# Kernel tuning notes

Hardware: AMD Instinct MI355X
Metric: run time of the kernel (lower is better)

The kernel has to match this reference:

```python
import jax, jax.numpy as jnp
import numpy as np

N = 4096   # out_features (rows of W)
M = 4096   # in_features (cols of W)
S_L = 2048 # Givens pairs on rows
S_R = 2048 # Givens pairs on cols
T = 8192   # tokens (batch*seq)
EPS = 1e-6


def _disjoint_pairs(key, n_feat, n_pairs):
    perm = jax.random.permutation(key, n_feat)[: 2 * n_pairs]
    return perm.reshape(n_pairs, 2).astype(jnp.int32)


def setup_inputs() -> dict:
    key = jax.random.key(0)
    ks = jax.random.split(key, 8)
    x = jax.random.normal(ks[0], (T, M), dtype=jnp.float32)
    W = 0.02 * jax.random.normal(ks[1], (N, M), dtype=jnp.float32)
    bias = jnp.zeros((N,), dtype=jnp.float32)
    theta_L = 0.002 * jax.random.normal(ks[2], (S_L,), dtype=jnp.float32)
    theta_R = 0.002 * jax.random.normal(ks[3], (S_R,), dtype=jnp.float32)
    pairs_L = _disjoint_pairs(ks[4], N, S_L)
    pairs_R = _disjoint_pairs(ks[5], M, S_R)
    ecd_log_mag = jnp.zeros((N,), dtype=jnp.float32)
    base_row_norms = jnp.linalg.norm(W, axis=1)  # [N], captured at init
    return {"x": x, "W": W, "bias": bias, "theta_L": theta_L,
            "theta_R": theta_R, "ecd_log_mag": ecd_log_mag,
            "base_row_norms": base_row_norms, "pairs_L": pairs_L,
            "pairs_R": pairs_R}


def _rotate_rows(Wm, pairs, theta):
    # Disjoint Givens rotations on rows: gather pair rows, 2x2 rotate, scatter.
    i, j = pairs[:, 0], pairs[:, 1]
    c = jnp.cos(theta)[:, None]
    s = jnp.sin(theta)[:, None]
    ri, rj = Wm[i], Wm[j]              # [S, M] gathers
    return Wm.at[i].set(c * ri - s * rj).at[j].set(s * ri + c * rj)


def _rotate_cols(Wm, pairs, theta):
    i, j = pairs[:, 0], pairs[:, 1]
    c = jnp.cos(theta)[None, :]
    s = jnp.sin(theta)[None, :]
    ci, cj = Wm[:, i], Wm[:, j]        # [N, S] gathers
    return Wm.at[:, i].set(c * ci - s * cj).at[:, j].set(s * ci + c * cj)


def reference(x, W, bias, theta_L, theta_R, ecd_log_mag, base_row_norms,
              pairs_L, pairs_R):
    # Effective weight: W_eff = G_L(theta_L) @ W @ G_R(theta_R)^T
    W_eff = _rotate_rows(_rotate_cols(W, pairs_R, theta_R), pairs_L, theta_L)
    # Magnitude (ECD) rescaling: restore base per-row norms modulated by
    # learned log-magnitudes.
    row_norms = jnp.sqrt(jnp.sum(W_eff * W_eff, axis=1) + EPS)  # [N]
    scale = base_row_norms * jnp.exp(ecd_log_mag) / row_norms   # [N]
    W_eff = W_eff * scale[:, None]
    return x @ W_eff.T + bias
```

## Files before the change

### kernel.cpp

```cpp
#include <hip/hip_runtime.h>
#include <cstdint>
#include <cstddef>

constexpr int T_N = 8192;
constexpr int MM  = 4096;
constexpr int NN  = 4096;
constexpr int S_L = 2048;
constexpr int S_R = 2048;
constexpr float EPS_ = 1e-6f;

typedef float  f32x4   __attribute__((ext_vector_type(4)));
typedef __bf16 bf16x8  __attribute__((ext_vector_type(8)));
typedef unsigned short ushort8 __attribute__((ext_vector_type(8)));

__device__ __forceinline__ unsigned short f2bf(float f) {
  unsigned int u = __float_as_uint(f);
  u += 0x7FFFu + ((u >> 16) & 1u);
  return (unsigned short)(u >> 16);
}

__global__ void init_cols(float* colC, float* colS, int* colP) {
  int i = blockIdx.x * blockDim.x + threadIdx.x;
  if (i < MM) { colC[i] = 1.f; colS[i] = 0.f; colP[i] = i; }
}

__global__ void build_cols(const float* __restrict__ thR, const int* __restrict__ prR,
                           float* colC, float* colS, int* colP) {
  int s = blockIdx.x * blockDim.x + threadIdx.x;
  if (s < S_R) {
    int i = prR[2*s], j = prR[2*s+1];
    float c = cosf(thR[s]), sn = sinf(thR[s]);
    colC[i] = c; colS[i] = -sn; colP[i] = j;
    colC[j] = c; colS[j] =  sn; colP[j] = i;
  }
}

__global__ __launch_bounds__(256) void weff_conv(
    const float* __restrict__ W, const float* __restrict__ brn, const float* __restrict__ elm,
    const float* __restrict__ thL, const int* __restrict__ prL,
    const float* __restrict__ colC, const float* __restrict__ colS, const int* __restrict__ colP,
    unsigned short* __restrict__ Wb,
    const float* __restrict__ x, unsigned short* __restrict__ xb)
{
  __shared__ __align__(16) float rI[MM];
  __shared__ __align__(16) float rJ[MM];
  __shared__ float red[8];

  int bid = blockIdx.x;
  int tid = threadIdx.x;

  if (bid >= S_L) {
    const size_t total = (size_t)T_N * MM / 8;
    for (size_t i = (size_t)(bid - S_L) * 256 + tid; i < total; i += 2048ull * 256ull) {
      const float* s = x + i * 8;
      f32x4 v0 = *(const f32x4*)s;
      f32x4 v1 = *(const f32x4*)(s + 4);
      ushort8 p;
      p[0] = f2bf(v0.x); p[1] = f2bf(v0.y); p[2] = f2bf(v0.z); p[3] = f2bf(v0.w);
      p[4] = f2bf(v1.x); p[5] = f2bf(v1.y); p[6] = f2bf(v1.z); p[7] = f2bf(v1.w);
      *(ushort8*)(xb + i * 8) = p;
    }
    return;
  }

  int s = bid;
  int i = prL[2*s], j = prL[2*s+1];
  float cl = cosf(thL[s]), sl = sinf(thL[s]);
  const float* Wi = W + (size_t)i * MM;
  const float* Wj = W + (size_t)j * MM;

  for (int m = tid * 4; m < MM; m += 1024) {
    *(f32x4*)&rI[m] = *(const f32x4*)&Wi[m];
    *(f32x4*)&rJ[m] = *(const f32x4*)&Wj[m];
  }
  __syncthreads();

  float ssi = 0.f, ssj = 0.f;
  for (int m = tid; m < MM; m += 256) {
    int p = colP[m];
    float c = colC[m], sn = colS[m];
    float vi = c * rI[m] + sn * rI[p];
    float vj = c * rJ[m] + sn * rJ[p];
    float ei = cl * vi - sl * vj;
    float ej = sl * vi + cl * vj;
    ssi += ei * ei;
    ssj += ej * ej;
  }
  #pragma unroll
  for (int o = 32; o; o >>= 1) { ssi += __shfl_xor(ssi, o); ssj += __shfl_xor(ssj, o); }
  int lane = tid & 63, wid = tid >> 6;
  if (lane == 0) { red[wid] = ssi; red[4 + wid] = ssj; }
  __syncthreads();
  float ti = red[0] + red[1] + red[2] + red[3];
  float tj = red[4] + red[5] + red[6] + red[7];
  float sci = brn[i] * expf(elm[i]) / sqrtf(ti + EPS_);
  float scj = brn[j] * expf(elm[j]) / sqrtf(tj + EPS_);

  for (int m0 = tid * 8; m0 < MM; m0 += 2048) {
    ushort8 pi, pj;
    #pragma unroll
    for (int q = 0; q < 8; q++) {
      int m = m0 + q;
      int p = colP[m];
      float c = colC[m], sn = colS[m];
      float vi = c * rI[m] + sn * rI[p];
      float vj = c * rJ[m] + sn * rJ[p];
      pi[q] = f2bf((cl * vi - sl * vj) * sci);
      pj[q] = f2bf((sl * vi + cl * vj) * scj);
    }
    *(ushort8*)&Wb[(size_t)i * MM + m0] = pi;
    *(ushort8*)&Wb[(size_t)j * MM + m0] = pj;
  }
}

typedef const __attribute__((address_space(1))) unsigned int* as1_u32p;
typedef __attribute__((address_space(3))) unsigned int* as3_u32p;

__device__ __forceinline__ void gl_lds16(const void* g, void* l) {
  __builtin_amdgcn_global_load_lds((as1_u32p)g, (as3_u32p)l, 16, 0, 0);
}

constexpr int GBM = 256, GBN = 256, GBK = 64;
constexpr int NTK = MM / GBK;
constexpr int BUFB = GBM * GBK * 2;

#define SB0() __builtin_amdgcn_sched_barrier(0)
#define BAR() __builtin_amdgcn_s_barrier()
#define LGKM(N) do { asm volatile("s_waitcnt lgkmcnt(" #N ")" ::: "memory"); \
                     SB0(); } while (0)

#define RD_A8(DST, AB, MIH)                                                   \
  _Pragma("unroll") for (int i_ = 0; i_ < 4; ++i_)                            \
  _Pragma("unroll") for (int k_ = 0; k_ < 2; ++k_)                            \
    DST[i_][k_] = *(const bf16x8*)((AB) + arow0 + ((MIH) * 4 + i_) * 2048     \
                                    + ((k_ * 64 + lg * 16) ^ sw));

#define RD_B4(DST, BB, NIH)                                                   \
  _Pragma("unroll") for (int n_ = 0; n_ < 2; ++n_)                            \
  _Pragma("unroll") for (int k_ = 0; k_ < 2; ++k_)                            \
    DST[n_][k_] = *(const bf16x8*)((BB) + brow0 + ((NIH) * 2 + n_) * 2048     \
                                    + ((k_ * 64 + lg * 16) ^ sw));

#define QMF(AF, BF, MI0, NI0)                                                 \
  __builtin_amdgcn_s_setprio(1);                                              \
  _Pragma("unroll") for (int k_ = 0; k_ < 2; ++k_)                            \
  _Pragma("unroll") for (int i_ = 0; i_ < 4; ++i_)                            \
  _Pragma("unroll") for (int n_ = 0; n_ < 2; ++n_)                            \
    acc[(MI0) + i_][(NI0) + n_] = __builtin_amdgcn_mfma_f32_16x16x32_bf16(    \
        AF[i_][k_], BF[n_][k_], acc[(MI0) + i_][(NI0) + n_], 0, 0, 0);        \
  __builtin_amdgcn_s_setprio(0);

#define STG_A(KOF, BUF, H)                                                    \
  _Pragma("unroll") for (int l_ = 2 * (H); l_ < 2 * (H) + 2; ++l_)            \
    gl_lds16(sA + (size_t)l_ * (64 * MM) + (KOF),                             \
             ldsA + (BUF) * BUFB + dstb + l_ * 8192);
#define STG_B(KOF, BUF, H)                                                    \
  _Pragma("unroll") for (int l_ = 2 * (H); l_ < 2 * (H) + 2; ++l_)            \
    gl_lds16(sB + (size_t)l_ * (64 * MM) + (KOF),                             \
             ldsB + (BUF) * BUFB + dstb + l_ * 8192);

#define GATE6  asm volatile("s_waitcnt vmcnt(6)" ::: "memory")
#define GATE0v asm volatile("s_waitcnt vmcnt(0)" ::: "memory")
#define GNONE  do { } while (0)
#define NOST   do { } while (0)

#define TILE4(T, BB, ST1, ST2, ST3, ST4, GATE)                                \
  {                                                                           \
    const char* Ab_ = ldsA + (BB) * BUFB;                                     \
    const char* Bb_ = ldsB + (BB) * BUFB;                                     \
    bf16x8 a0[4][2], a1[4][2], b0[2][2], b1[2][2];                            \
                          \
    RD_B4(b0, Bb_, 0);                                                        \
    RD_A8(a0, Ab_, 0);                                                        \
    SB0();                                                                    \
    ST1;                                                                      \
    LGKM(8);                                                                  \
    BAR();                                                                    \
    LGKM(0);                                                                  \
    QMF(a0, b0, 0, 0);                                                        \
    BAR();                                                                    \
                                    \
    RD_A8(a1, Ab_, 1);                                                        \
    SB0();                                                                    \
    ST2;                                                                      \
    BAR();                                                                    \
    LGKM(0);                                                                  \
    QMF(a1, b0, 4, 0);                                                        \
    BAR();                                                                    \
                                    \
    RD_B4(b1, Bb_, 1);                                                        \
    SB0();                                                                    \
    ST3;                                                                      \
    BAR();                                                                    \
    LGKM(0);                                                                  \
    QMF(a1, b1, 4, 2);                                                        \
    BAR();                                                                    \
                  \
    ST4;                                                                      \
    GATE;                                                                     \
    BAR();                                                                    \
    QMF(a0, b1, 0, 2);                                                        \
    BAR();                                                                    \
  }

__global__ __launch_bounds__(512, 2) void gemm8(
    const unsigned short* __restrict__ xb,
    const unsigned short* __restrict__ wb,
    const float* __restrict__ bias,
    float* __restrict__ C)
{
  __shared__ __align__(16) unsigned short As[2 * GBM * GBK];
  __shared__ __align__(16) unsigned short Bs[2 * GBN * GBK];
  char* ldsA = (char*)As;
  char* ldsB = (char*)Bs;

  int bid = blockIdx.x;
  int swz = (bid & 7) * 64 + (bid >> 3);
  int tn = swz & 15, tm = swz >> 4;
  const int trow0 = tm * GBM;
  const int tcol0 = tn * GBN;

  int tid  = threadIdx.x;
  int lane = tid & 63;
  int wid  = tid >> 6;
  int wr = wid >> 2, wc = wid & 3;
  int lr = lane & 15;
  int lg = lane >> 4;
  const int sw = (lr & 7) << 4;
  const int arow0 = (wr * 128 + lr) * 128;
  const int brow0 = (wc * 64  + lr) * 128;

  const int r0   = tid >> 3;
  const int colg = (tid & 7) ^ (r0 & 7);
  const unsigned short* sA = xb + (size_t)(trow0 + r0) * MM + colg * 8;
  const unsigned short* sB = wb + (size_t)(tcol0 + r0) * MM + colg * 8;
  const int dstb = tid * 16;

  f32x4 acc[8][4];
  #pragma unroll
  for (int i = 0; i < 8; i++)
    #pragma unroll
    for (int j = 0; j < 4; j++) {
      f32x4 z = {0.f, 0.f, 0.f, 0.f};
      acc[i][j] = z;
    }

  STG_A(0, 0, 0); STG_A(0, 0, 1); STG_B(0, 0, 0); STG_B(0, 0, 1);
  STG_A(GBK, 1, 0); STG_A(GBK, 1, 1); STG_B(GBK, 1, 0);
  asm volatile("s_waitcnt vmcnt(6)" ::: "memory");
  __builtin_amdgcn_s_barrier();

  #pragma unroll 1
  for (int t = 0; t < NTK - 2; t += 2) {
    TILE4(t, 0,
          STG_B((t + 1) * GBK, 1, 1),
          STG_A((t + 2) * GBK, 0, 0),
          STG_A((t + 2) * GBK, 0, 1),
          STG_B((t + 2) * GBK, 0, 0),
          GATE6);
    TILE4(t + 1, 1,
          STG_B((t + 2) * GBK, 0, 1),
          STG_A((t + 3) * GBK, 1, 0),
          STG_A((t + 3) * GBK, 1, 1),
          STG_B((t + 3) * GBK, 1, 0),
          GATE6);
  }
  TILE4(NTK - 2, 0,
        STG_B((NTK - 1) * GBK, 1, 1),
        NOST, NOST, NOST, GATE0v);
  TILE4(NTK - 1, 1, NOST, NOST, NOST, NOST, GNONE);

  #pragma unroll
  for (int ni = 0; ni < 4; ++ni) {
    int col = tcol0 + wc * 64 + ni * 16 + lr;
    float bi = bias[col];
    #pragma unroll
    for (int mi = 0; mi < 8; ++mi) {
      int rr0 = trow0 + wr * 128 + mi * 16 + lg * 4;
      #pragma unroll
      for (int qq = 0; qq < 4; ++qq)
        C[(size_t)(rr0 + qq) * NN + col] = acc[mi][ni][qq] + bi;
    }
  }
}

constexpr int BM = 128, BN = 128, BK = 64;

__global__ __launch_bounds__(256) void gemm_fb(
    const float* __restrict__ xf,
    const unsigned short* __restrict__ wb, const float* __restrict__ bias,
    float* __restrict__ C)
{
  __shared__ __align__(16) unsigned short As2[BM * BK];
  __shared__ __align__(16) unsigned short Bs2[BN * BK];

  int bid = blockIdx.x;
  int swz = (bid & 7) * 256 + (bid >> 3);
  int tn = swz & 31;
  int tm = swz >> 5;

  int tid  = threadIdx.x;
  int lane = tid & 63;
  int wid  = tid >> 6;
  int wr = wid >> 1, wc = wid & 1;
  int lr = lane & 15;
  int lg = lane >> 4;

  f32x4 acc[4][4];
  #pragma unroll
  for (int i = 0; i < 4; i++)
    #pragma unroll
    for (int j = 0; j < 4; j++) {
      f32x4 z = {0.f, 0.f, 0.f, 0.f};
      acc[i][j] = z;
    }

  int srow = tid >> 3;
  int scol = (tid & 7) * 8;
  const size_t a_base = (size_t)(tm * BM) * MM;
  const size_t b_base = (size_t)(tn * BN) * MM;

  for (int k0 = 0; k0 < MM; k0 += BK) {
    #pragma unroll
    for (int c = 0; c < 4; c++) {
      int row = c * 32 + srow;
      gl_lds16(wb + b_base + (size_t)row * MM + k0 + scol,
               (char*)Bs2 + (c * 256 + wid * 64) * 16);
    }
    #pragma unroll
    for (int c = 0; c < 4; c++) {
      int row = c * 32 + srow;
      const float* s = xf + a_base + (size_t)row * MM + k0 + scol;
      f32x4 v0 = *(const f32x4*)s;
      f32x4 v1 = *(const f32x4*)(s + 4);
      ushort8 p;
      p[0] = f2bf(v0.x); p[1] = f2bf(v0.y); p[2] = f2bf(v0.z); p[3] = f2bf(v0.w);
      p[4] = f2bf(v1.x); p[5] = f2bf(v1.y); p[6] = f2bf(v1.z); p[7] = f2bf(v1.w);
      *(ushort8*)&As2[(c * 256 + tid) * 8] = p;
    }
    __syncthreads();

    #pragma unroll
    for (int kk = 0; kk < 2; kk++) {
      bf16x8 a[4], b[4];
      #pragma unroll
      for (int i = 0; i < 4; i++) {
        a[i] = *(const bf16x8*)&As2[(wr * 64 + i * 16 + lr) * BK + kk * 32 + lg * 8];
        b[i] = *(const bf16x8*)&Bs2[(wc * 64 + i * 16 + lr) * BK + kk * 32 + lg * 8];
      }
      #pragma unroll
      for (int i = 0; i < 4; i++)
        #pragma unroll
        for (int j = 0; j < 4; j++)
          acc[i][j] = __builtin_amdgcn_mfma_f32_16x16x32_bf16(a[i], b[j], acc[i][j], 0, 0, 0);
    }
    __syncthreads();
  }

  int gn0 = tn * BN + wc * 64;
  int gt0 = tm * BM + wr * 64;
  #pragma unroll
  for (int j = 0; j < 4; j++) {
    int gn = gn0 + j * 16 + lr;
    float bi = bias[gn];
    #pragma unroll
    for (int i = 0; i < 4; i++) {
      int t0 = gt0 + i * 16 + lg * 4;
      #pragma unroll
      for (int q = 0; q < 4; q++)
        C[(size_t)(t0 + q) * NN + gn] = acc[i][j][q] + bi;
    }
  }
}

extern "C" void kernel_launch(void* const* d_in, const int* in_sizes, int n_in,
                              void* d_out, int out_size, void* d_ws, size_t ws_size,
                              hipStream_t stream)
{
  const float* x    = (const float*)d_in[0];
  const float* W    = (const float*)d_in[1];
  const float* bias = (const float*)d_in[2];
  const float* thL  = (const float*)d_in[3];
  const float* thR  = (const float*)d_in[4];
  const float* elm  = (const float*)d_in[5];
  const float* brn  = (const float*)d_in[6];
  const int*   prL  = (const int*)d_in[7];
  const int*   prR  = (const int*)d_in[8];
  float* out = (float*)d_out;

  char* ws = (char*)d_ws;
  unsigned short* Wb = (unsigned short*)ws;
  size_t off = (size_t)NN * MM * 2;
  float* colC = (float*)(ws + off); off += MM * 4;
  float* colS = (float*)(ws + off); off += MM * 4;
  int*   colP = (int*)  (ws + off); off += MM * 4;
  unsigned short* xb = (unsigned short*)(ws + off);
  bool use_xb = ws_size >= off + (size_t)T_N * MM * 2;

  init_cols <<<16, 256, 0, stream>>>(colC, colS, colP);
  build_cols<<< 8, 256, 0, stream>>>(thR, prR, colC, colS, colP);

  if (use_xb) {
    weff_conv<<<S_L + 2048, 256, 0, stream>>>(W, brn, elm, thL, prL,
                                              colC, colS, colP, Wb, x, xb);
    gemm8<<<512, 512, 0, stream>>>(xb, Wb, bias, out);
  } else {
    weff_conv<<<S_L, 256, 0, stream>>>(W, brn, elm, thL, prL,
                                       colC, colS, colP, Wb, x, xb);
    gemm_fb<<<2048, 256, 0, stream>>>(x, Wb, bias, out);
  }
}
```

Baseline: 302.0 us.

## Prefetch next tile's first A/B fragments during the current tile's MFMAs

Restructures the GEMM main loop so the a0/b0 LDS fragments for the next k-tile are read during the last MFMA phase of the current tile, using double-buffered register sets. LDS reads now overlap with MFMA work instead of stalling at the start of each tile. Global-to-LDS staging is reordered around this, and the vmcnt gate moves from 6 to 4. The cost is extra register pressure from holding two fragment sets, which could hurt occupancy at 2 waves per SIMD, plus more delicate ordering across the barriers.

```diff
diff --git a/kernel.cpp b/kernel.cpp
--- a/kernel.cpp
+++ b/kernel.cpp
@@ -126,7 +126,7 @@
 
 #define SB0() __builtin_amdgcn_sched_barrier(0)
 #define BAR() __builtin_amdgcn_s_barrier()
-#define LGKM(N) do { asm volatile("s_waitcnt lgkmcnt(" #N ")" ::: "memory"); \
+#define LGKM0() do { asm volatile("s_waitcnt lgkmcnt(0)" ::: "memory"); \
                      SB0(); } while (0)
 
 #define RD_A8(DST, AB, MIH)                                                   \
@@ -159,47 +159,41 @@
     gl_lds16(sB + (size_t)l_ * (64 * MM) + (KOF),                             \
              ldsB + (BUF) * BUFB + dstb + l_ * 8192);
 
-#define GATE6  asm volatile("s_waitcnt vmcnt(6)" ::: "memory")
-#define GATE0v asm volatile("s_waitcnt vmcnt(0)" ::: "memory")
+#define GATE4x asm volatile("s_waitcnt vmcnt(4)" ::: "memory")
+#define GATE0x asm volatile("s_waitcnt vmcnt(0)" ::: "memory")
 #define GNONE  do { } while (0)
-#define NOST   do { } while (0)
-
-#define TILE4(T, BB, ST1, ST2, ST3, ST4, GATE)                                \
+
+#define TILEX(T, BB, a0C, b0C, a0N, b0N, DOB1, DOT2, GATE3, DORDN)            \
   {                                                                           \
-    const char* Ab_ = ldsA + (BB) * BUFB;                                     \
-    const char* Bb_ = ldsB + (BB) * BUFB;                                     \
-    bf16x8 a0[4][2], a1[4][2], b0[2][2], b1[2][2];                            \
-                          \
-    RD_B4(b0, Bb_, 0);                                                        \
-    RD_A8(a0, Ab_, 0);                                                        \
-    SB0();                                                                    \
-    ST1;                                                                      \
-    LGKM(8);                                                                  \
-    BAR();                                                                    \
-    LGKM(0);                                                                  \
-    QMF(a0, b0, 0, 0);                                                        \
-    BAR();                                                                    \
-                                    \
+    const char* Ab_  = ldsA + (BB) * BUFB;                                    \
+    const char* Bb_  = ldsB + (BB) * BUFB;                                    \
+    const char* AbN_ = ldsA + ((BB) ^ 1) * BUFB;                              \
+    const char* BbN_ = ldsB + ((BB) ^ 1) * BUFB;                              \
+    bf16x8 a1[4][2], b1[2][2];                                                \
+                         \
+    LGKM0();                                                                  \
     RD_A8(a1, Ab_, 1);                                                        \
     SB0();                                                                    \
-    ST2;                                                                      \
+    QMF(a0C, b0C, 0, 0);                                                      \
+    if (DOB1) { STG_B(((T) + 1) * GBK, (BB) ^ 1, 1); }                        \
     BAR();                                                                    \
-    LGKM(0);                                                                  \
-    QMF(a1, b0, 4, 0);                                                        \
-    BAR();                                                                    \
-                                    \
+                            \
+    LGKM0();                                                                  \
     RD_B4(b1, Bb_, 1);                                                        \
     SB0();                                                                    \
-    ST3;                                                                      \
+    QMF(a1, b0C, 4, 0);                                                       \
+    if (DOT2) { STG_B(((T) + 2) * GBK, (BB), 0); }                            \
     BAR();                                                                    \
-    LGKM(0);                                                                  \
+                            \
+    LGKM0();                                                                  \
     QMF(a1, b1, 4, 2);                                                        \
+    if (DOT2) { STG_A(((T) + 2) * GBK, (BB), 0); }                            \
+    GATE3;                                                                    \
     BAR();                                                                    \
-                  \
-    ST4;                                                                      \
-    GATE;                                                                     \
-    BAR();                                                                    \
-    QMF(a0, b1, 0, 2);                                                        \
+                 \
+    if (DORDN) { RD_B4(b0N, BbN_, 0); RD_A8(a0N, AbN_, 0); SB0(); }           \
+    QMF(a0C, b1, 0, 2);                                                       \
+    if (DOT2) { STG_A(((T) + 2) * GBK, (BB), 1); }                            \
     BAR();                                                                    \
   }
 
@@ -246,29 +240,21 @@
     }
 
   STG_A(0, 0, 0); STG_A(0, 0, 1); STG_B(0, 0, 0); STG_B(0, 0, 1);
-  STG_A(GBK, 1, 0); STG_A(GBK, 1, 1); STG_B(GBK, 1, 0);
+  STG_B(GBK, 1, 0); STG_A(GBK, 1, 0); STG_A(GBK, 1, 1);
   asm volatile("s_waitcnt vmcnt(6)" ::: "memory");
   __builtin_amdgcn_s_barrier();
 
+  bf16x8 a0A[4][2], b0A[2][2], a0B[4][2], b0B[2][2];
+  RD_B4(b0A, ldsB, 0);
+  RD_A8(a0A, ldsA, 0);
+
   #pragma unroll 1
   for (int t = 0; t < NTK - 2; t += 2) {
-    TILE4(t, 0,
-          STG_B((t + 1) * GBK, 1, 1),
-          STG_A((t + 2) * GBK, 0, 0),
-          STG_A((t + 2) * GBK, 0, 1),
-          STG_B((t + 2) * GBK, 0, 0),
-          GATE6);
-    TILE4(t + 1, 1,
-          STG_B((t + 2) * GBK, 0, 1),
-          STG_A((t + 3) * GBK, 1, 0),
-          STG_A((t + 3) * GBK, 1, 1),
-          STG_B((t + 3) * GBK, 1, 0),
-          GATE6);
-  }
-  TILE4(NTK - 2, 0,
-        STG_B((NTK - 1) * GBK, 1, 1),
-        NOST, NOST, NOST, GATE0v);
-  TILE4(NTK - 1, 1, NOST, NOST, NOST, NOST, GNONE);
+    TILEX(t,     0, a0A, b0A, a0B, b0B, 1, 1, GATE4x, 1);
+    TILEX(t + 1, 1, a0B, b0B, a0A, b0A, 1, 1, GATE4x, 1);
+  }
+  TILEX(NTK - 2, 0, a0A, b0A, a0B, b0B, 1, 0, GATE0x, 1);
+  TILEX(NTK - 1, 1, a0B, b0B, a0A, b0A, 0, 0, GNONE, 0);
 
   #pragma unroll
   for (int ni = 0; ni < 4; ++ni) {
```

After: 312.1 us. 3.3% more time.
